# Kernel optimization log

Hardware: AMD Instinct MI355X
Metric: run time of the kernel (lower is better)

## Reference

```python
import jax, jax.numpy as jnp
import numpy as np

TOKENS = 32768
HIDDEN = 2048
N_EXPERTS = 128
TOP_K = 8
NORM_TOPK_PROB = True


def setup_inputs() -> dict:
    key = jax.random.key(0)
    k1, k2 = jax.random.split(key)
    hidden_states = jax.random.normal(k1, (TOKENS, HIDDEN), dtype=jnp.float32)
    # router weight [num_experts, hidden_dim]; small init like a trained gate
    weight = jax.random.normal(k2, (N_EXPERTS, HIDDEN), dtype=jnp.float32) * 0.02
    return {"hidden_states": hidden_states, "weight": weight}


def reference(hidden_states, weight):
    # flatten tokens (already [T, H])
    x = hidden_states.reshape(-1, HIDDEN)
    # router logits: [T, E]
    logits = jnp.einsum("th,eh->te", x, weight)
    # softmax in float32 (matches dtype=torch.float)
    probs = jax.nn.softmax(logits.astype(jnp.float32), axis=-1)
    # top-k over experts
    top_val, top_idx = jax.lax.top_k(probs, TOP_K)  # [T, K], [T, K]
    if NORM_TOPK_PROB:
        top_val = top_val / jnp.sum(top_val, axis=-1, keepdims=True)
    top_val = top_val.astype(probs.dtype)
    # scatter renormalized weights into dense [T, E] score tensor
    rows = jnp.arange(x.shape[0])[:, None]  # [T, 1]
    scores = jnp.zeros_like(probs).at[rows, top_idx].set(top_val)
    return scores, top_idx
```

## Files before the change

kernel.cpp:

```cpp
#include <hip/hip_runtime.h>
#include <hip/hip_bf16.h>

#define NT   32768
#define NH   2048
#define NE   128
#define TOPK 8
#define BT   32
#define BND    6.0e-4f
#define TWO_B  (2.0f * BND)

#define WS_W_OFF   64
#define WS_REC_U32 262160

typedef __attribute__((ext_vector_type(8))) short bf16x8;
typedef __attribute__((ext_vector_type(4))) float f32x4;
typedef __attribute__((ext_vector_type(4))) unsigned int u32x4;

static __device__ __forceinline__ unsigned short f2bf(float f) {
    __hip_bfloat16 h = __float2bfloat16(f);
    return *reinterpret_cast<unsigned short*>(&h);
}

__global__ __launch_bounds__(256) void prep_w_kernel(
    const float* __restrict__ W, unsigned short* __restrict__ Wt)
{
    int g = blockIdx.x * 256 + threadIdx.x;
    int lane = g & 63;
    int te   = (g >> 6) & 7;
    int s    = (g >> 9) & 1;
    int k32  = g >> 10;
    int row  = te * 16 + (lane & 15);
    int kb   = k32 * 32 + (lane >> 4) * 8;
    const float* src = W + (size_t)row * NH + kb;
    float4 f0 = *(const float4*)src;
    float4 f1 = *(const float4*)(src + 4);
    float f[8] = {f0.x, f0.y, f0.z, f0.w, f1.x, f1.y, f1.z, f1.w};
    bf16x8 o;
    #pragma unroll
    for (int e = 0; e < 8; ++e) {
        unsigned short h = f2bf(f[e]);
        if (s == 0) o[e] = (short)h;
        else {
            float fh = __builtin_bit_cast(float, ((unsigned int)h) << 16);
            o[e] = (short)f2bf(f[e] - fh);
        }
    }
    *(bf16x8*)(Wt + (size_t)g * 8) = o;
}

__global__ __launch_bounds__(256, 2) void router_gemm_kernel(
    const float* __restrict__ X, const unsigned short* __restrict__ Wt,
    float* __restrict__ outLg)
{
    __shared__ float ps[2][BT * 132];

    const int tid  = threadIdx.x;
    const int lane = tid & 63;
    const int w    = tid >> 6;
    const int l15  = lane & 15, lhi = lane >> 4;
    const int t0   = blockIdx.x * BT;

    f32x4 acc[2][8];
    #pragma unroll
    for (int i = 0; i < 2; ++i)
        #pragma unroll
        for (int te = 0; te < 8; ++te) acc[i][te] = (f32x4){0.f, 0.f, 0.f, 0.f};

    const float* x0 = X + (size_t)(t0 + l15) * NH + w * 512 + lhi * 8;
    const float* x1 = x0 + 16 * NH;
    const unsigned short* wbase = Wt + (size_t)(w * 16) * 8192 + lane * 8;

    bf16x8 b0[8][2], b1[8][2];

    #define LOADB(arr, kk) do {                                                \
        const unsigned short* wb_ = wbase + (size_t)(kk) * 8192;               \
        _Pragma("unroll")                                                      \
        for (int te = 0; te < 8; ++te) {                                       \
            arr[te][0] = *(const bf16x8*)(wb_ + te * 512);                     \
            arr[te][1] = *(const bf16x8*)(wb_ + 4096 + te * 512);              \
        }                                                                      \
    } while (0)

    #define SPLITA(kk, ah, al) do {                                            \
        _Pragma("unroll")                                                      \
        for (int i = 0; i < 2; ++i) {                                          \
            const float* xp = (i ? x1 : x0) + (kk) * 32;                       \
            float4 fa = *(const float4*)xp;                                    \
            float4 fb = *(const float4*)(xp + 4);                              \
            float ff[8] = {fa.x, fa.y, fa.z, fa.w, fb.x, fb.y, fb.z, fb.w};    \
            unsigned int hu[4], lu[4];                                         \
            _Pragma("unroll")                                                  \
            for (int p = 0; p < 4; ++p) {                                      \
                unsigned int u0 = __builtin_bit_cast(unsigned int, ff[2*p]);   \
                unsigned int u1 = __builtin_bit_cast(unsigned int, ff[2*p+1]); \
                unsigned int r0 = u0 + 0x8000u, r1 = u1 + 0x8000u;             \
                hu[p] = (r0 >> 16) | (r1 & 0xFFFF0000u);                       \
                float h0 = __builtin_bit_cast(float, r0 & 0xFFFF0000u);        \
                float h1 = __builtin_bit_cast(float, r1 & 0xFFFF0000u);        \
                float e0 = ff[2*p] - h0, e1 = ff[2*p+1] - h1;                  \
                unsigned int s0 = __builtin_bit_cast(unsigned int, e0) + 0x8000u; \
                unsigned int s1 = __builtin_bit_cast(unsigned int, e1) + 0x8000u; \
                lu[p] = (s0 >> 16) | (s1 & 0xFFFF0000u);                       \
            }                                                                  \
            ah[i] = __builtin_bit_cast(bf16x8, (u32x4){hu[0],hu[1],hu[2],hu[3]}); \
            al[i] = __builtin_bit_cast(bf16x8, (u32x4){lu[0],lu[1],lu[2],lu[3]}); \
        }                                                                      \
    } while (0)

    #define DOMFMA(b, ah, al) do {                                             \
        _Pragma("unroll")                                                      \
        for (int te = 0; te < 8; ++te) {                                       \
            acc[0][te] = __builtin_amdgcn_mfma_f32_16x16x32_bf16(ah[0], b[te][0], acc[0][te], 0, 0, 0); \
            acc[1][te] = __builtin_amdgcn_mfma_f32_16x16x32_bf16(ah[1], b[te][0], acc[1][te], 0, 0, 0); \
            acc[0][te] = __builtin_amdgcn_mfma_f32_16x16x32_bf16(al[0], b[te][0], acc[0][te], 0, 0, 0); \
            acc[1][te] = __builtin_amdgcn_mfma_f32_16x16x32_bf16(al[1], b[te][0], acc[1][te], 0, 0, 0); \
            acc[0][te] = __builtin_amdgcn_mfma_f32_16x16x32_bf16(ah[0], b[te][1], acc[0][te], 0, 0, 0); \
            acc[1][te] = __builtin_amdgcn_mfma_f32_16x16x32_bf16(ah[1], b[te][1], acc[1][te], 0, 0, 0); \
        }                                                                      \
    } while (0)

    LOADB(b0, 0);
    for (int p = 0; p < 8; ++p) {
        bf16x8 ah[2], al[2];
        LOADB(b1, 2 * p + 1);
        SPLITA(2 * p, ah, al);
        DOMFMA(b0, ah, al);
        if (p < 7) LOADB(b0, 2 * p + 2);
        SPLITA(2 * p + 1, ah, al);
        DOMFMA(b1, ah, al);
    }

    if (w < 2) {
        #pragma unroll
        for (int i = 0; i < 2; ++i)
            #pragma unroll
            for (int te = 0; te < 8; ++te)
                #pragma unroll
                for (int q = 0; q < 4; ++q)
                    ps[w][(i * 16 + lhi * 4 + q) * 132 + te * 16 + l15] = acc[i][te][q];
    }
    __syncthreads();
    if (w >= 2) {
        #pragma unroll
        for (int i = 0; i < 2; ++i)
            #pragma unroll
            for (int te = 0; te < 8; ++te)
                #pragma unroll
                for (int q = 0; q < 4; ++q) {
                    int o = (i * 16 + lhi * 4 + q) * 132 + te * 16 + l15;
                    ps[w - 2][o] += acc[i][te][q];
                }
    }
    __syncthreads();
    #pragma unroll
    for (int q = 0; q < 4; ++q) {
        int i = tid + q * 256;
        int row = i >> 5, c4 = i & 31;
        int o = row * 132 + c4 * 4;
        float4 a = *(float4*)&ps[0][o];
        float4 b = *(float4*)&ps[1][o];
        a.x += b.x; a.y += b.y; a.z += b.z; a.w += b.w;
        *(float4*)(outLg + (size_t)(t0 + row) * NE + c4 * 4) = a;
    }
}

__global__ __launch_bounds__(256) void select_kernel(
    float* out, unsigned int* __restrict__ ws)
{
    const int lane   = threadIdx.x & 63;
    const int wid    = (blockIdx.x * (blockDim.x >> 6)) + (threadIdx.x >> 6);
    const int nwaves = gridDim.x * (blockDim.x >> 6);

    for (int t = wid; t < NT; t += nwaves) {
        float* row = out + (size_t)t * NE;
        float2 v2 = *(const float2*)(row + lane * 2);
        const float ov0 = v2.x, ov1 = v2.y;
        float v0 = ov0, v1 = ov1;
        const int i0 = lane * 2, i1 = lane * 2 + 1;

        float myv = 0.f; int myi = 0;
        int r0 = -1, r1 = -1;

        #pragma unroll
        for (int k = 0; k < 13; ++k) {
            float av = v0; int ai = i0;
            if (v1 > av) { av = v1; ai = i1; }
            #pragma unroll
            for (int off = 32; off >= 1; off >>= 1) {
                float qv = __shfl_xor(av, off);
                int   qi = __shfl_xor(ai, off);
                if (qv > av || (qv == av && qi < ai)) { av = qv; ai = qi; }
            }
            if (lane == k) { myv = av; myi = ai; }
            if (k < 8) {
                if (i0 == ai) r0 = k;
                if (i1 == ai) r1 = k;
            }
            if (i0 == ai) v0 = -3.0e38f;
            if (i1 == ai) v1 = -3.0e38f;
        }

        const float top0 = __shfl(myv, 0);
        const float v7   = __shfl(myv, 7);
        const float v12  = __shfl(myv, 12);
        const float nv   = __shfl(myv, lane + 1);

        const bool gap = (lane < 8) && (myv - nv < TWO_B);
        const bool flagged = __any(gap);

        float pvk = (lane < 8) ? expf(myv - top0) : 0.f;
        float ksum = pvk;
        #pragma unroll
        for (int off = 1; off < 8; off <<= 1) ksum += __shfl_xor(ksum, off);
        ksum = __shfl(ksum, lane & 56);
        ksum = __shfl(ksum, 0);

        float o0 = 0.f, o1 = 0.f;
        if (r0 >= 0) o0 = expf(ov0 - top0) / ksum;
        if (r1 >= 0) o1 = expf(ov1 - top0) / ksum;
        *(float2*)(row + lane * 2) = make_float2(o0, o1);

        if (lane < 8)
            out[(size_t)NT * NE + (size_t)t * TOPK + lane] = (float)myi;

        if (flagged) {
            const float thr = v7 - TWO_B;
            unsigned int cnt;
            if (v12 >= thr) {
                cnt = 0xFFu;
            } else {
                bool inc = (lane < 8) || (lane < 13 && myv >= thr);
                cnt = (unsigned int)__popcll(__ballot(inc) & 0x1FFFull);
            }
            unsigned int wrd0 = 0, wrd1 = 0, wrd2 = 0, wrd3 = 0;
            #pragma unroll
            for (int b = 0; b < 4; ++b) {
                unsigned int id;
                id = (unsigned int)__shfl(myi, 0 + b)  & 255u;
                if ((unsigned int)(0 + b)  < cnt) wrd0 |= id << (8 * b);
                id = (unsigned int)__shfl(myi, 4 + b)  & 255u;
                if ((unsigned int)(4 + b)  < cnt) wrd1 |= id << (8 * b);
                id = (unsigned int)__shfl(myi, 8 + b)  & 255u;
                if ((unsigned int)(8 + b)  < cnt && cnt != 0xFFu) wrd2 |= id << (8 * b);
                id = (unsigned int)__shfl(myi, 12 + b) & 255u;
                if ((unsigned int)(12 + b) < cnt && cnt != 0xFFu) wrd3 |= id << (8 * b);
            }
            if (lane == 0) {
                unsigned int slot = atomicAdd(ws, 1u);
                unsigned int* rec = ws + WS_REC_U32 + slot * 8;
                rec[0] = (unsigned int)t;
                rec[1] = cnt;
                rec[2] = wrd0; rec[3] = wrd1; rec[4] = wrd2; rec[5] = wrd3;
            }
        }
    }
}

__global__ __launch_bounds__(256) void finalize_kernel(
    const float* __restrict__ X, const float* __restrict__ W,
    float* __restrict__ out, const unsigned int* __restrict__ ws)
{
    __shared__ float  xs[2048];
    __shared__ double cv[128];
    __shared__ int    cid[128];
    __shared__ float  ovals[8];
    __shared__ int    oidx[8];

    const int tid = threadIdx.x;
    const int lane = tid & 63, w = tid >> 6;
    const unsigned int n = ws[0];

    for (unsigned int rI = blockIdx.x; rI < n; rI += gridDim.x) {
        const unsigned int* rec = ws + WS_REC_U32 + rI * 8;
        const int tg = (int)rec[0];
        const unsigned int cnt = rec[1];
        const unsigned char* ids = (const unsigned char*)(rec + 2);
        const int nc = (cnt == 0xFFu) ? NE : (int)cnt;

        #pragma unroll
        for (int q = 0; q < 2; ++q) {
            int i = tid + q * 256;
            *(float4*)(xs + i * 4) = *(const float4*)(X + (size_t)tg * NH + i * 4);
        }
        __syncthreads();

        for (int c = w; c < nc; c += 4) {
            int e = (cnt == 0xFFu) ? c : (int)ids[c];
            const float* wrow = W + (size_t)e * NH;
            double s = 0.0;
            #pragma unroll
            for (int m = 0; m < 8; ++m) {
                float4 wv = *(const float4*)(wrow + m * 256 + lane * 4);
                float4 xv = *(const float4*)(xs + m * 256 + lane * 4);
                s = fma((double)xv.x, (double)wv.x, s);
                s = fma((double)xv.y, (double)wv.y, s);
                s = fma((double)xv.z, (double)wv.z, s);
                s = fma((double)xv.w, (double)wv.w, s);
            }
            #pragma unroll
            for (int off = 32; off >= 1; off >>= 1) s += __shfl_xor(s, off);
            if (lane == 0) { cv[c] = s; cid[c] = e; }
        }
        __syncthreads();

        if (tid == 0) {
            double lv[8];
            #pragma unroll
            for (int k = 0; k < 8; ++k) {
                double best = -1.0e300; int bi = 1 << 30, bc = 0;
                for (int c = 0; c < nc; ++c) {
                    double v = cv[c]; int e = cid[c];
                    if (v > best || (v == best && e < bi)) { best = v; bi = e; bc = c; }
                }
                lv[k] = best; oidx[k] = bi; cv[bc] = -1.0e301;
            }
            double m = lv[0], sum = 0.0, p[8];
            #pragma unroll
            for (int k = 0; k < 8; ++k) { p[k] = exp(lv[k] - m); sum += p[k]; }
            #pragma unroll
            for (int k = 0; k < 8; ++k) ovals[k] = (float)(p[k] / sum);
        }
        __syncthreads();

        float* srow = out + (size_t)tg * NE;
        if (tid < NE) {
            float val = 0.f;
            #pragma unroll
            for (int k = 0; k < 8; ++k) if (oidx[k] == tid) val = ovals[k];
            srow[tid] = val;
        }
        if (tid < TOPK) out[(size_t)NT * NE + (size_t)tg * TOPK + tid] = (float)oidx[tid];
        __syncthreads();
    }
}

extern "C" void kernel_launch(void* const* d_in, const int* in_sizes, int n_in,
                              void* d_out, int out_size, void* d_ws, size_t ws_size,
                              hipStream_t stream) {
    const float* X = (const float*)d_in[0];
    const float* W = (const float*)d_in[1];
    float* out = (float*)d_out;
    unsigned char* wsb = (unsigned char*)d_ws;
    unsigned short* Wt = (unsigned short*)(wsb + WS_W_OFF);

    hipMemsetAsync(d_ws, 0, 64, stream);
    prep_w_kernel<<<256, 256, 0, stream>>>(W, Wt);
    router_gemm_kernel<<<NT / BT, 256, 0, stream>>>(X, Wt, out);
    select_kernel<<<2048, 256, 0, stream>>>(out, (unsigned int*)d_ws);
    finalize_kernel<<<1024, 256, 0, stream>>>(X, W, out, (const unsigned int*)d_ws);
}
```

Baseline: 236.5 us.

## Fuse top-k selection into router GEMM with larger 128-token tiles

Merges the softmax/top-k select pass into the GEMM kernel, which now reads logits from shared memory instead of writing them to global memory and reading them back. The token tile grows from 32 to 128 with 512-thread blocks (8 waves: 2 token groups by 4 K-splits), so each W fragment load is reused across 4 token subtiles, and the K-split reduction goes through LDS. The explicit double-buffered B loads are replaced by a simpler loop with unroll 2. The risks are lower occupancy (one block of 512 per CU, large accumulator arrays), fewer blocks (256), and serialized LDS reduction steps.

```diff
diff --git a/kernel.cpp b/kernel.cpp
--- a/kernel.cpp
+++ b/kernel.cpp
@@ -5,7 +5,7 @@
 #define NH   2048
 #define NE   128
 #define TOPK 8
-#define BT   32
+#define BTOK 128
 #define BND    6.0e-4f
 #define TWO_B  (2.0f * BND)
 
@@ -48,131 +48,90 @@
     *(bf16x8*)(Wt + (size_t)g * 8) = o;
 }
 
-__global__ __launch_bounds__(256, 2) void router_gemm_kernel(
+__global__ __launch_bounds__(512, 1) void router_gemm_kernel(
     const float* __restrict__ X, const unsigned short* __restrict__ Wt,
-    float* __restrict__ outLg)
+    float* out, unsigned int* __restrict__ ws)
 {
-    __shared__ float ps[2][BT * 132];
+    __shared__ float ps[BTOK * 132];
 
     const int tid  = threadIdx.x;
     const int lane = tid & 63;
-    const int w    = tid >> 6;
+    const int wv   = tid >> 6;
+    const int g    = wv & 1;
+    const int h    = wv >> 1;
     const int l15  = lane & 15, lhi = lane >> 4;
-    const int t0   = blockIdx.x * BT;
-
-    f32x4 acc[2][8];
+    const int t0   = blockIdx.x * BTOK;
+
+    f32x4 acc[4][8];
     #pragma unroll
-    for (int i = 0; i < 2; ++i)
+    for (int i = 0; i < 4; ++i)
         #pragma unroll
         for (int te = 0; te < 8; ++te) acc[i][te] = (f32x4){0.f, 0.f, 0.f, 0.f};
 
-    const float* x0 = X + (size_t)(t0 + l15) * NH + w * 512 + lhi * 8;
-    const float* x1 = x0 + 16 * NH;
-    const unsigned short* wbase = Wt + (size_t)(w * 16) * 8192 + lane * 8;
-
-    bf16x8 b0[8][2], b1[8][2];
-
-    #define LOADB(arr, kk) do {                                                \
-        const unsigned short* wb_ = wbase + (size_t)(kk) * 8192;               \
-        _Pragma("unroll")                                                      \
-        for (int te = 0; te < 8; ++te) {                                       \
-            arr[te][0] = *(const bf16x8*)(wb_ + te * 512);                     \
-            arr[te][1] = *(const bf16x8*)(wb_ + 4096 + te * 512);              \
-        }                                                                      \
-    } while (0)
-
-    #define SPLITA(kk, ah, al) do {                                            \
-        _Pragma("unroll")                                                      \
-        for (int i = 0; i < 2; ++i) {                                          \
-            const float* xp = (i ? x1 : x0) + (kk) * 32;                       \
-            float4 fa = *(const float4*)xp;                                    \
-            float4 fb = *(const float4*)(xp + 4);                              \
-            float ff[8] = {fa.x, fa.y, fa.z, fa.w, fb.x, fb.y, fb.z, fb.w};    \
-            unsigned int hu[4], lu[4];                                         \
-            _Pragma("unroll")                                                  \
-            for (int p = 0; p < 4; ++p) {                                      \
-                unsigned int u0 = __builtin_bit_cast(unsigned int, ff[2*p]);   \
-                unsigned int u1 = __builtin_bit_cast(unsigned int, ff[2*p+1]); \
-                unsigned int r0 = u0 + 0x8000u, r1 = u1 + 0x8000u;             \
-                hu[p] = (r0 >> 16) | (r1 & 0xFFFF0000u);                       \
-                float h0 = __builtin_bit_cast(float, r0 & 0xFFFF0000u);        \
-                float h1 = __builtin_bit_cast(float, r1 & 0xFFFF0000u);        \
-                float e0 = ff[2*p] - h0, e1 = ff[2*p+1] - h1;                  \
-                unsigned int s0 = __builtin_bit_cast(unsigned int, e0) + 0x8000u; \
-                unsigned int s1 = __builtin_bit_cast(unsigned int, e1) + 0x8000u; \
-                lu[p] = (s0 >> 16) | (s1 & 0xFFFF0000u);                       \
-            }                                                                  \
-            ah[i] = __builtin_bit_cast(bf16x8, (u32x4){hu[0],hu[1],hu[2],hu[3]}); \
-            al[i] = __builtin_bit_cast(bf16x8, (u32x4){lu[0],lu[1],lu[2],lu[3]}); \
-        }                                                                      \
-    } while (0)
-
-    #define DOMFMA(b, ah, al) do {                                             \
-        _Pragma("unroll")                                                      \
-        for (int te = 0; te < 8; ++te) {                                       \
-            acc[0][te] = __builtin_amdgcn_mfma_f32_16x16x32_bf16(ah[0], b[te][0], acc[0][te], 0, 0, 0); \
-            acc[1][te] = __builtin_amdgcn_mfma_f32_16x16x32_bf16(ah[1], b[te][0], acc[1][te], 0, 0, 0); \
-            acc[0][te] = __builtin_amdgcn_mfma_f32_16x16x32_bf16(al[0], b[te][0], acc[0][te], 0, 0, 0); \
-            acc[1][te] = __builtin_amdgcn_mfma_f32_16x16x32_bf16(al[1], b[te][0], acc[1][te], 0, 0, 0); \
-            acc[0][te] = __builtin_amdgcn_mfma_f32_16x16x32_bf16(ah[0], b[te][1], acc[0][te], 0, 0, 0); \
-            acc[1][te] = __builtin_amdgcn_mfma_f32_16x16x32_bf16(ah[1], b[te][1], acc[1][te], 0, 0, 0); \
-        }                                                                      \
-    } while (0)
-
-    LOADB(b0, 0);
-    for (int p = 0; p < 8; ++p) {
-        bf16x8 ah[2], al[2];
-        LOADB(b1, 2 * p + 1);
-        SPLITA(2 * p, ah, al);
-        DOMFMA(b0, ah, al);
-        if (p < 7) LOADB(b0, 2 * p + 2);
-        SPLITA(2 * p + 1, ah, al);
-        DOMFMA(b1, ah, al);
-    }
-
-    if (w < 2) {
-        #pragma unroll
-        for (int i = 0; i < 2; ++i)
-            #pragma unroll
-            for (int te = 0; te < 8; ++te)
+    const float* xb = X + (size_t)(t0 + g * 64 + l15) * NH + h * 512 + lhi * 8;
+    const unsigned short* wq = Wt + (size_t)(h * 16) * 8192 + lane * 8;
+
+    #pragma unroll 2
+    for (int kk = 0; kk < 16; ++kk) {
+        bf16x8 ah[4], al[4];
+        #pragma unroll
+        for (int i = 0; i < 4; ++i) {
+            const float* xp = xb + (size_t)i * 16 * NH + kk * 32;
+            float4 fa = *(const float4*)xp;
+            float4 fb = *(const float4*)(xp + 4);
+            float ff[8] = {fa.x, fa.y, fa.z, fa.w, fb.x, fb.y, fb.z, fb.w};
+            unsigned int hu[4], lu[4];
+            #pragma unroll
+            for (int p = 0; p < 4; ++p) {
+                unsigned int u0 = __builtin_bit_cast(unsigned int, ff[2 * p]);
+                unsigned int u1 = __builtin_bit_cast(unsigned int, ff[2 * p + 1]);
+                unsigned int r0 = u0 + 0x8000u, r1 = u1 + 0x8000u;
+                hu[p] = (r0 >> 16) | (r1 & 0xFFFF0000u);
+                float h0 = __builtin_bit_cast(float, r0 & 0xFFFF0000u);
+                float h1 = __builtin_bit_cast(float, r1 & 0xFFFF0000u);
+                float e0 = ff[2 * p] - h0, e1 = ff[2 * p + 1] - h1;
+                unsigned int s0 = __builtin_bit_cast(unsigned int, e0) + 0x8000u;
+                unsigned int s1 = __builtin_bit_cast(unsigned int, e1) + 0x8000u;
+                lu[p] = (s0 >> 16) | (s1 & 0xFFFF0000u);
+            }
+            ah[i] = __builtin_bit_cast(bf16x8, (u32x4){hu[0], hu[1], hu[2], hu[3]});
+            al[i] = __builtin_bit_cast(bf16x8, (u32x4){lu[0], lu[1], lu[2], lu[3]});
+        }
+        const unsigned short* wb = wq + (size_t)kk * 8192;
+        #pragma unroll
+        for (int te = 0; te < 8; ++te) {
+            bf16x8 bh = *(const bf16x8*)(wb + te * 512);
+            bf16x8 bl = *(const bf16x8*)(wb + 4096 + te * 512);
+            #pragma unroll
+            for (int i = 0; i < 4; ++i) {
+                acc[i][te] = __builtin_amdgcn_mfma_f32_16x16x32_bf16(ah[i], bh, acc[i][te], 0, 0, 0);
+                acc[i][te] = __builtin_amdgcn_mfma_f32_16x16x32_bf16(al[i], bh, acc[i][te], 0, 0, 0);
+                acc[i][te] = __builtin_amdgcn_mfma_f32_16x16x32_bf16(ah[i], bl, acc[i][te], 0, 0, 0);
+            }
+        }
+    }
+
+    #pragma unroll
+    for (int s = 0; s < 4; ++s) {
+        if (h == s) {
+            #pragma unroll
+            for (int i = 0; i < 4; ++i)
                 #pragma unroll
-                for (int q = 0; q < 4; ++q)
-                    ps[w][(i * 16 + lhi * 4 + q) * 132 + te * 16 + l15] = acc[i][te][q];
-    }
-    __syncthreads();
-    if (w >= 2) {
-        #pragma unroll
-        for (int i = 0; i < 2; ++i)
-            #pragma unroll
-            for (int te = 0; te < 8; ++te)
-                #pragma unroll
-                for (int q = 0; q < 4; ++q) {
-                    int o = (i * 16 + lhi * 4 + q) * 132 + te * 16 + l15;
-                    ps[w - 2][o] += acc[i][te][q];
-                }
-    }
-    __syncthreads();
-    #pragma unroll
-    for (int q = 0; q < 4; ++q) {
-        int i = tid + q * 256;
-        int row = i >> 5, c4 = i & 31;
-        int o = row * 132 + c4 * 4;
-        float4 a = *(float4*)&ps[0][o];
-        float4 b = *(float4*)&ps[1][o];
-        a.x += b.x; a.y += b.y; a.z += b.z; a.w += b.w;
-        *(float4*)(outLg + (size_t)(t0 + row) * NE + c4 * 4) = a;
-    }
-}
-
-__global__ __launch_bounds__(256) void select_kernel(
-    float* out, unsigned int* __restrict__ ws)
-{
-    const int lane   = threadIdx.x & 63;
-    const int wid    = (blockIdx.x * (blockDim.x >> 6)) + (threadIdx.x >> 6);
-    const int nwaves = gridDim.x * (blockDim.x >> 6);
-
-    for (int t = wid; t < NT; t += nwaves) {
-        float* row = out + (size_t)t * NE;
+                for (int te = 0; te < 8; ++te)
+                    #pragma unroll
+                    for (int q = 0; q < 4; ++q) {
+                        int o = (g * 64 + i * 16 + lhi * 4 + q) * 132 + te * 16 + l15;
+                        if (s == 0) ps[o] = acc[i][te][q];
+                        else        ps[o] += acc[i][te][q];
+                    }
+        }
+        __syncthreads();
+    }
+
+    for (int j = 0; j < 16; ++j) {
+        const int tl = wv * 16 + j;
+        const int tg = t0 + tl;
+        const float* row = &ps[tl * 132];
         float2 v2 = *(const float2*)(row + lane * 2);
         const float ov0 = v2.x, ov1 = v2.y;
         float v0 = ov0, v1 = ov1;
@@ -208,20 +167,18 @@
         const bool gap = (lane < 8) && (myv - nv < TWO_B);
         const bool flagged = __any(gap);
 
-        float pvk = (lane < 8) ? expf(myv - top0) : 0.f;
-        float ksum = pvk;
+        float ksum = (lane < 8) ? expf(myv - top0) : 0.f;
         #pragma unroll
         for (int off = 1; off < 8; off <<= 1) ksum += __shfl_xor(ksum, off);
-        ksum = __shfl(ksum, lane & 56);
         ksum = __shfl(ksum, 0);
 
         float o0 = 0.f, o1 = 0.f;
         if (r0 >= 0) o0 = expf(ov0 - top0) / ksum;
         if (r1 >= 0) o1 = expf(ov1 - top0) / ksum;
-        *(float2*)(row + lane * 2) = make_float2(o0, o1);
+        *(float2*)(out + (size_t)tg * NE + lane * 2) = make_float2(o0, o1);
 
         if (lane < 8)
-            out[(size_t)NT * NE + (size_t)t * TOPK + lane] = (float)myi;
+            out[(size_t)NT * NE + (size_t)tg * TOPK + lane] = (float)myi;
 
         if (flagged) {
             const float thr = v7 - TWO_B;
@@ -248,7 +205,7 @@
             if (lane == 0) {
                 unsigned int slot = atomicAdd(ws, 1u);
                 unsigned int* rec = ws + WS_REC_U32 + slot * 8;
-                rec[0] = (unsigned int)t;
+                rec[0] = (unsigned int)tg;
                 rec[1] = cnt;
                 rec[2] = wrd0; rec[3] = wrd1; rec[4] = wrd2; rec[5] = wrd3;
             }
@@ -345,7 +302,6 @@
 
     hipMemsetAsync(d_ws, 0, 64, stream);
     prep_w_kernel<<<256, 256, 0, stream>>>(W, Wt);
-    router_gemm_kernel<<<NT / BT, 256, 0, stream>>>(X, Wt, out);
-    select_kernel<<<2048, 256, 0, stream>>>(out, (unsigned int*)d_ws);
+    router_gemm_kernel<<<NT / BTOK, 512, 0, stream>>>(X, Wt, out, (unsigned int*)d_ws);
     finalize_kernel<<<1024, 256, 0, stream>>>(X, W, out, (const unsigned int*)d_ws);
 }
```

Measured after the change: 271.5 us. +14.8%, slower.
